# Optimization experiments

Hardware: AMD Instinct MI355X
Metric: run time of the kernel (lower is better)

The kernel has to match this reference:

```python
import jax, jax.numpy as jnp
import numpy as np

N_NODES = 50000
N_EDGES = 600000
N_GRAPHS = 64
D_NODE = 64
D_EDGE = 16
HID = 128
N_LAYERS = 3
LN_EPS = 1e-5


def setup_inputs() -> dict:
    key = jax.random.key(0)
    ks = jax.random.split(key, 16)
    inp = {
        'x': jax.random.normal(ks[0], (N_NODES, D_NODE), dtype=jnp.float32),
        'edge_index': jax.random.randint(ks[1], (2, N_EDGES), 0, N_NODES, dtype=jnp.int64),
        'edge_attr': jax.random.normal(ks[2], (N_EDGES, D_EDGE), dtype=jnp.float32),
        'batch': jnp.sort(jax.random.randint(ks[3], (N_NODES,), 0, N_GRAPHS, dtype=jnp.int64)),
    }
    def lin(k, fan_in, fan_out):
        bound = 1.0 / np.sqrt(fan_in)
        kw, kb = jax.random.split(k)
        w = jax.random.uniform(kw, (fan_in, fan_out), minval=-bound, maxval=bound, dtype=jnp.float32)
        b = jax.random.uniform(kb, (fan_out,), minval=-bound, maxval=bound, dtype=jnp.float32)
        return w, b
    inp['enc_w'], inp['enc_b'] = lin(ks[4], D_NODE, HID)
    inp['ln_g'] = jnp.ones((HID,), jnp.float32)
    inp['ln_b'] = jnp.zeros((HID,), jnp.float32)
    inp['edge_w'], inp['edge_b'] = lin(ks[5], D_EDGE, HID // 2)
    cw, cb = [], []
    for i in range(N_LAYERS):
        w, b = lin(ks[6 + i], HID, HID)
        cw.append(w); cb.append(b)
    inp['conv_ws'] = jnp.stack(cw)  # [L, HID, HID]
    inp['conv_bs'] = jnp.stack(cb)  # [L, HID]
    inp['c1_w'], inp['c1_b'] = lin(ks[10], HID, HID // 2)
    inp['c2_w'], inp['c2_b'] = lin(ks[11], HID // 2, 1)
    return inp


def _layernorm(h, g, b):
    mu = jnp.mean(h, axis=-1, keepdims=True)
    var = jnp.mean(jnp.square(h - mu), axis=-1, keepdims=True)
    return (h - mu) * jax.lax.rsqrt(var + LN_EPS) * g + b


def _gcn_forward(x, edge_attr, batch, src, dst,
                 enc_w, enc_b, ln_g, ln_b, edge_w, edge_b,
                 conv_ws, conv_bs, c1_w, c1_b, c2_w, c2_b):
    # node encoder: Linear -> ReLU -> LayerNorm
    h = _layernorm(jax.nn.relu(x @ enc_w + enc_b), ln_g, ln_b)
    # edge encoder (output unused downstream, kept for fidelity)
    _ = jax.nn.relu(edge_attr @ edge_w + edge_b)
    # GCN normalization with self-loops: deg = in-degree + 1
    deg = jax.ops.segment_sum(jnp.ones((src.shape[0],), h.dtype), dst, num_segments=N_NODES) + 1.0
    dis = jax.lax.rsqrt(deg)  # deg >= 1
    edge_norm = (dis[src] * dis[dst])[:, None]
    self_norm = (dis * dis)[:, None]  # 1/deg for self-loop
    for i in range(N_LAYERS):
        hw = h @ conv_ws[i]
        agg = jax.ops.segment_sum(hw[src] * edge_norm, dst, num_segments=N_NODES)
        h = agg + hw * self_norm + conv_bs[i]
        h = jax.nn.relu(h)  # dropout is identity at eval
    # global mean pool over graphs
    sums = jax.ops.segment_sum(h, batch, num_segments=N_GRAPHS)
    cnts = jax.ops.segment_sum(jnp.ones((h.shape[0],), h.dtype), batch, num_segments=N_GRAPHS)
    pooled = sums / jnp.maximum(cnts, 1.0)[:, None]
    # classifier: Linear -> ReLU -> (Dropout) -> Linear
    return jax.nn.relu(pooled @ c1_w + c1_b) @ c2_w + c2_b


def reference(x, edge_index, edge_attr, batch, enc_w, enc_b, ln_g, ln_b,
              edge_w, edge_b, conv_ws, conv_bs, c1_w, c1_b, c2_w, c2_b):
    src, dst = edge_index[0], edge_index[1]
    return _gcn_forward(x, edge_attr, batch, src, dst, enc_w, enc_b, ln_g, ln_b,
                        edge_w, edge_b, conv_ws, conv_bs, c1_w, c1_b, c2_w, c2_b)
```

## Files before the change

kernel.cpp:

```cpp
#include <hip/hip_runtime.h>

#define HID 128
#define DNODE 64
#define NNODES 50000
#define NEDGES 600000
#define NGRAPHS 64
#define LN_EPS 1e-5f

#define NBUCK 782
#define EPB 4096
#define BK1 ((NEDGES + EPB - 1) / EPB)

#define NZERO (NBUCK + NGRAPHS * HID)
#define NZERO4 ((NZERO + 3) / 4)
#define Z_BLKS ((NZERO4 + 255) / 256)
#define PKWC_BLKS (3 * 16384 / 256)
#define PKWE_BLKS (8192 / 256)
#define BND_BLKS ((NNODES + 255) / 256)

#define ENC_BLKS ((NNODES + 63) / 64)
#define E256_BLKS ((NEDGES + 255) / 256)

#define GC_BLKS (NNODES / 16)

typedef __attribute__((ext_vector_type(8))) short bf16x8;
typedef __attribute__((ext_vector_type(8))) unsigned short u16x8;
typedef __attribute__((ext_vector_type(4))) float f32x4;
typedef __attribute__((ext_vector_type(2))) float f32x2;

static __device__ __forceinline__ unsigned short f2bf(float f) {
  unsigned int u = __float_as_uint(f);
  u += 0x7fffu + ((u >> 16) & 1u);
  return (unsigned short)(u >> 16);
}
static __device__ __forceinline__ float bf2f(unsigned short h) {
  return __uint_as_float(((unsigned int)h) << 16);
}
static __device__ __forceinline__ void fp8x4_to_f32(unsigned int w, float* o) {
  f32x2 lo = __builtin_amdgcn_cvt_pk_f32_fp8(w, false);
  f32x2 hi = __builtin_amdgcn_cvt_pk_f32_fp8(w, true);
  o[0] = lo[0]; o[1] = lo[1]; o[2] = hi[0]; o[3] = hi[1];
}
static __device__ __forceinline__ unsigned int f32x4_to_fp8(float a, float b,
                                                            float c, float d) {
  unsigned int v = __builtin_amdgcn_cvt_pk_fp8_f32(a, b, 0, false);
  v = __builtin_amdgcn_cvt_pk_fp8_f32(c, d, v, true);
  return v;
}

__global__ void __launch_bounds__(256) prep0_kernel(
    int4* __restrict__ zp, const float* __restrict__ W,
    unsigned short* __restrict__ Wp, const float* __restrict__ enc_w,
    unsigned short* __restrict__ Wpe, const int* __restrict__ batch,
    int* __restrict__ gstart, int* __restrict__ gend) {
  int b = blockIdx.x;
  if (b < Z_BLKS) {
    int i = b * 256 + threadIdx.x;
    if (i < NZERO4) zp[i] = make_int4(0, 0, 0, 0);
  } else if (b < Z_BLKS + PKWC_BLKS) {
    int t = (b - Z_BLKS) * 256 + threadIdx.x;
    int i = t & 7;
    int lane = (t >> 3) & 63;
    int kk = (t >> 9) & 3;
    int nt = (t >> 11) & 7;
    int layer = t >> 14;
    int k = kk * 32 + (lane >> 4) * 8 + i;
    int n = nt * 16 + (lane & 15);
    Wp[t] = f2bf(W[((size_t)layer * HID + k) * HID + n]);
  } else if (b < Z_BLKS + PKWC_BLKS + PKWE_BLKS) {
    int t = (b - Z_BLKS - PKWC_BLKS) * 256 + threadIdx.x;
    int i = t & 7;
    int lane = (t >> 3) & 63;
    int kk = (t >> 9) & 1;
    int nt = (t >> 10) & 7;
    int k = kk * 32 + (lane >> 4) * 8 + i;
    int n = nt * 16 + (lane & 15);
    Wpe[t] = f2bf(enc_w[(size_t)k * HID + n]);
  } else {
    int i = (b - Z_BLKS - PKWC_BLKS - PKWE_BLKS) * 256 + threadIdx.x;
    if (i < NNODES) {
      int g = batch[i];
      if (i == 0 || batch[i - 1] != g) gstart[g] = i;
      if (i == NNODES - 1 || batch[i + 1] != g) gend[g] = i + 1;
    }
  }
}

__global__ void __launch_bounds__(256) prep1_kernel(
    const float* __restrict__ x, const unsigned short* __restrict__ Wpe,
    const unsigned short* __restrict__ Wp0, const float* __restrict__ enc_b,
    const float* __restrict__ ln_g, const float* __restrict__ ln_b,
    unsigned char* __restrict__ B1, const int* __restrict__ dst,
    int* __restrict__ gcount, unsigned int* __restrict__ bpos) {
  __shared__ __align__(16) unsigned short tile[4][16][136];
  __shared__ int lhist[NBUCK];
  int blk = blockIdx.x;
  if (blk < BK1) {
    int t = threadIdx.x;
    for (int i = t; i < NBUCK; i += 256) lhist[i] = 0;
    __syncthreads();
    int base = blk * EPB;
    int myd[16];
    int myr[16];
#pragma unroll
    for (int i = 0; i < 16; ++i) {
      int e = base + i * 256 + t;
      if (e < NEDGES) {
        int d = dst[e];
        myd[i] = d;
        myr[i] = atomicAdd(&lhist[d >> 6], 1);
      } else {
        myd[i] = -1;
        myr[i] = 0;
      }
    }
    __syncthreads();
    for (int i = t; i < NBUCK; i += 256) {
      int c = lhist[i];
      if (c) lhist[i] = atomicAdd(&gcount[i], c);
    }
    __syncthreads();
#pragma unroll
    for (int i = 0; i < 16; ++i) {
      if (myd[i] >= 0) {
        int e = base + i * 256 + t;
        bpos[e] = (unsigned int)(lhist[myd[i] >> 6] + myr[i]);
      }
    }
    return;
  }
  int b2 = blk - BK1;
  int wave = threadIdx.x >> 6;
  int lane = threadIdx.x & 63;
  int l15 = lane & 15, h = lane >> 4;
  int base = b2 * 64 + wave * 16;
  int row = base + l15;
  int rowc = row < NNODES ? row : NNODES - 1;
  const float* xr = x + (size_t)rowc * DNODE;
  bf16x8 a[2];
#pragma unroll
  for (int kk = 0; kk < 2; ++kk) {
    float4 p0 = *(const float4*)(xr + kk * 32 + h * 8);
    float4 p1 = *(const float4*)(xr + kk * 32 + h * 8 + 4);
    a[kk][0] = (short)f2bf(p0.x); a[kk][1] = (short)f2bf(p0.y);
    a[kk][2] = (short)f2bf(p0.z); a[kk][3] = (short)f2bf(p0.w);
    a[kk][4] = (short)f2bf(p1.x); a[kk][5] = (short)f2bf(p1.y);
    a[kk][6] = (short)f2bf(p1.z); a[kk][7] = (short)f2bf(p1.w);
  }
  f32x4 acc[8];
#pragma unroll
  for (int nt = 0; nt < 8; ++nt) acc[nt] = (f32x4)(0.f);
  const bf16x8* wp = (const bf16x8*)Wpe;
#pragma unroll
  for (int kk = 0; kk < 2; ++kk)
#pragma unroll
    for (int nt = 0; nt < 8; ++nt)
      acc[nt] = __builtin_amdgcn_mfma_f32_16x16x32_bf16(a[kk], wp[(nt * 2 + kk) * 64 + lane],
                                                        acc[nt], 0, 0, 0);
  float s[4] = {0.f, 0.f, 0.f, 0.f}, s2[4] = {0.f, 0.f, 0.f, 0.f};
#pragma unroll
  for (int nt = 0; nt < 8; ++nt) {
    float bcol = enc_b[nt * 16 + l15];
#pragma unroll
    for (int r = 0; r < 4; ++r) {
      float v = fmaxf(acc[nt][r] + bcol, 0.f);
      acc[nt][r] = v;
      s[r] += v;
      s2[r] = fmaf(v, v, s2[r]);
    }
  }
#pragma unroll
  for (int r = 0; r < 4; ++r) {
#pragma unroll
    for (int o = 1; o < 16; o <<= 1) {
      s[r] += __shfl_xor(s[r], o);
      s2[r] += __shfl_xor(s2[r], o);
    }
  }
  float mu[4], rstd[4];
#pragma unroll
  for (int r = 0; r < 4; ++r) {
    mu[r] = s[r] * (1.0f / HID);
    float var = s2[r] * (1.0f / HID) - mu[r] * mu[r];
    rstd[r] = rsqrtf(var + LN_EPS);
  }
#pragma unroll
  for (int nt = 0; nt < 8; ++nt) {
    float gcol = ln_g[nt * 16 + l15], bbcol = ln_b[nt * 16 + l15];
#pragma unroll
    for (int r = 0; r < 4; ++r)
      tile[wave][h * 4 + r][nt * 16 + l15] =
          f2bf((acc[nt][r] - mu[r]) * rstd[r] * gcol + bbcol);
  }
  __syncthreads();
  bf16x8 a2[4];
#pragma unroll
  for (int kk = 0; kk < 4; ++kk)
    a2[kk] = *(const bf16x8*)&tile[wave][l15][kk * 32 + h * 8];
  __syncthreads();
  f32x4 acc2[8];
#pragma unroll
  for (int nt = 0; nt < 8; ++nt) acc2[nt] = (f32x4)(0.f);
#pragma unroll
  for (int kk = 0; kk < 4; ++kk) {
#pragma unroll
    for (int nt = 0; nt < 8; ++nt) {
      bf16x8 wf = *(const bf16x8*)(Wp0 + (((nt * 4 + kk) * 64 + lane) << 3));
      acc2[nt] = __builtin_amdgcn_mfma_f32_16x16x32_bf16(a2[kk], wf, acc2[nt], 0, 0, 0);
    }
  }
#pragma unroll
  for (int nt = 0; nt < 8; ++nt)
#pragma unroll
    for (int r = 0; r < 4; ++r)
      tile[wave][h * 4 + r][nt * 16 + l15] = f2bf(acc2[nt][r]);
  __syncthreads();
  int trow = lane >> 2, tseg = lane & 3;
  int orow = base + trow;
  if (orow < NNODES) {
#pragma unroll
    for (int q = 0; q < 4; ++q) {
      u16x8 v = *(const u16x8*)&tile[wave][trow][tseg * 32 + q * 8];
      uint2 o;
      o.x = f32x4_to_fp8(bf2f((unsigned short)v[0]), bf2f((unsigned short)v[1]),
                         bf2f((unsigned short)v[2]), bf2f((unsigned short)v[3]));
      o.y = f32x4_to_fp8(bf2f((unsigned short)v[4]), bf2f((unsigned short)v[5]),
                         bf2f((unsigned short)v[6]), bf2f((unsigned short)v[7]));
      *(uint2*)(B1 + (size_t)orow * HID + tseg * 32 + q * 8) = o;
    }
  }
}

__global__ void __launch_bounds__(1024) scan_kernel(
    const int* __restrict__ gcount, int* __restrict__ boff,
    int* __restrict__ off) {
  __shared__ int s[1024];
  int t = threadIdx.x;
  int v = (t < NBUCK) ? gcount[t] : 0;
  s[t] = v;
  __syncthreads();
  for (int d = 1; d < 1024; d <<= 1) {
    int xv = (t >= d) ? s[t - d] : 0;
    __syncthreads();
    s[t] += xv;
    __syncthreads();
  }
  if (t < NBUCK) boff[t] = s[t] - v;
  if (t == 0) {
    boff[NBUCK] = s[1023];
    off[NNODES] = NEDGES;
  }
}

__global__ void __launch_bounds__(256) scat_kernel(
    const int* __restrict__ src, const int* __restrict__ dst,
    const unsigned int* __restrict__ bpos, const int* __restrict__ boff,
    unsigned int* __restrict__ sorted1) {
  int e = blockIdx.x * 256 + threadIdx.x;
  if (e >= NEDGES) return;
  int d = dst[e];
  unsigned int u = ((unsigned int)d << 16) | (unsigned int)src[e];
  sorted1[boff[d >> 6] + bpos[e]] = u;
}

__global__ void __launch_bounds__(1024) bucket_kernel(
    const int* __restrict__ boff, const unsigned int* __restrict__ sorted1,
    int* __restrict__ off, float* __restrict__ dis,
    unsigned int* __restrict__ epack) {
  __shared__ int h64[64];
  __shared__ int cur[64];
  int b = blockIdx.x, t = threadIdx.x;
  int lo = boff[b], hi = boff[b + 1];
  if (t < 64) h64[t] = 0;
  __syncthreads();
  for (int i = lo + t; i < hi; i += 1024)
    atomicAdd(&h64[(sorted1[i] >> 16) & 63], 1);
  __syncthreads();
  if (t == 0) {
    int run = 0;
    for (int j = 0; j < 64; ++j) {
      int c = h64[j];
      cur[j] = lo + run;
      int n = b * 64 + j;
      if (n < NNODES) {
        off[n] = lo + run;
        dis[n] = rsqrtf((float)c + 1.0f);
      }
      run += c;
    }
  }
  __syncthreads();
  for (int i = lo + t; i < hi; i += 1024) {
    unsigned int u = sorted1[i];
    int p = atomicAdd(&cur[(u >> 16) & 63], 1);
    epack[p] = u;
  }
}

__global__ void __launch_bounds__(256) norm_kernel(
    const float* __restrict__ dis, unsigned int* __restrict__ epack) {
  int e = blockIdx.x * 256 + threadIdx.x;
  if (e >= NEDGES) return;
  unsigned int u = epack[e];
  int d = u >> 16;
  int sN = u & 0xFFFFu;
  epack[e] = ((unsigned int)f2bf(dis[sN] * dis[d]) << 16) | (unsigned int)sN;
}

__global__ void __launch_bounds__(1024) gc_kernel(
    const int* __restrict__ off, const unsigned int* __restrict__ epack,
    const float* __restrict__ dis, const float* __restrict__ bias,
    const unsigned char* __restrict__ Bin, const unsigned short* __restrict__ Wnext,
    unsigned char* __restrict__ Bout) {
  __shared__ __align__(16) unsigned short As[16][136];
  __shared__ __align__(16) unsigned short Bs[16][136];
  int w = threadIdx.x >> 6, lane = threadIdx.x & 63;
  int n = blockIdx.x * 16 + w;
  int slot = lane >> 4, p = lane & 15;
  int lo = off[n], hi = off[n + 1];
  float acc0[8], acc1[8];
#pragma unroll
  for (int i = 0; i < 8; ++i) { acc0[i] = 0.f; acc1[i] = 0.f; }
  int idx = lo + slot;
  for (; idx + 4 < hi; idx += 8) {
    unsigned int e0 = epack[idx];
    unsigned int e1 = epack[idx + 4];
    float w0 = bf2f((unsigned short)(e0 >> 16));
    float w1 = bf2f((unsigned short)(e1 >> 16));
    uint2 v0 = *(const uint2*)(Bin + (size_t)(e0 & 0xFFFFu) * HID + p * 8);
    uint2 v1 = *(const uint2*)(Bin + (size_t)(e1 & 0xFFFFu) * HID + p * 8);
    float f0[8], f1[8];
    fp8x4_to_f32(v0.x, f0); fp8x4_to_f32(v0.y, f0 + 4);
    fp8x4_to_f32(v1.x, f1); fp8x4_to_f32(v1.y, f1 + 4);
#pragma unroll
    for (int i = 0; i < 8; ++i) acc0[i] = fmaf(f0[i], w0, acc0[i]);
#pragma unroll
    for (int i = 0; i < 8; ++i) acc1[i] = fmaf(f1[i], w1, acc1[i]);
  }
  if (idx < hi) {
    unsigned int e0 = epack[idx];
    float w0 = bf2f((unsigned short)(e0 >> 16));
    uint2 v0 = *(const uint2*)(Bin + (size_t)(e0 & 0xFFFFu) * HID + p * 8);
    float f0[8];
    fp8x4_to_f32(v0.x, f0); fp8x4_to_f32(v0.y, f0 + 4);
#pragma unroll
    for (int i = 0; i < 8; ++i) acc0[i] = fmaf(f0[i], w0, acc0[i]);
  }
#pragma unroll
  for (int i = 0; i < 8; ++i) {
    float a = acc0[i] + acc1[i];
    a += __shfl_xor(a, 16);
    a += __shfl_xor(a, 32);
    acc0[i] = a;
  }
  if (slot == 0) {
    float dn = dis[n];
    float d2 = dn * dn;
    uint2 sv = *(const uint2*)(Bin + (size_t)n * HID + p * 8);
    float sf[8];
    fp8x4_to_f32(sv.x, sf); fp8x4_to_f32(sv.y, sf + 4);
    float4 b0 = ((const float4*)bias)[p * 2];
    float4 b1 = ((const float4*)bias)[p * 2 + 1];
    float bb[8] = {b0.x, b0.y, b0.z, b0.w, b1.x, b1.y, b1.z, b1.w};
    u16x8 o;
#pragma unroll
    for (int i = 0; i < 8; ++i) {
      float v = fmaxf(fmaf(sf[i], d2, bb[i]) + acc0[i], 0.f);
      o[i] = (short)f2bf(v);
    }
    *(u16x8*)&As[w][p * 8] = o;
  }
  __syncthreads();
  if (w < 8) {
    bf16x8 a[4];
#pragma unroll
    for (int kk = 0; kk < 4; ++kk)
      a[kk] = *(const bf16x8*)&As[p][kk * 32 + slot * 8];
    f32x4 acc = (f32x4)(0.f);
#pragma unroll
    for (int kk = 0; kk < 4; ++kk) {
      bf16x8 wf = *(const bf16x8*)(Wnext + (((w * 4 + kk) * 64 + lane) << 3));
      acc = __builtin_amdgcn_mfma_f32_16x16x32_bf16(a[kk], wf, acc, 0, 0, 0);
    }
#pragma unroll
    for (int r = 0; r < 4; ++r)
      Bs[slot * 4 + r][w * 16 + p] = f2bf(acc[r]);
  }
  __syncthreads();
  if (threadIdx.x < 256) {
    int row = threadIdx.x >> 4, seg = threadIdx.x & 15;
    u16x8 v = *(const u16x8*)&Bs[row][seg * 8];
    uint2 o;
    o.x = f32x4_to_fp8(bf2f((unsigned short)v[0]), bf2f((unsigned short)v[1]),
                       bf2f((unsigned short)v[2]), bf2f((unsigned short)v[3]));
    o.y = f32x4_to_fp8(bf2f((unsigned short)v[4]), bf2f((unsigned short)v[5]),
                       bf2f((unsigned short)v[6]), bf2f((unsigned short)v[7]));
    *(uint2*)(Bout + (size_t)(blockIdx.x * 16 + row) * HID + seg * 8) = o;
  }
}

__global__ void __launch_bounds__(1024) g2pool_kernel(
    const int* __restrict__ off, const unsigned int* __restrict__ epack,
    const float* __restrict__ dis, const float* __restrict__ bias,
    const unsigned char* __restrict__ Bin, const int* __restrict__ batch,
    float* __restrict__ sums) {
  __shared__ float Ps[16][132];
  __shared__ int bg[16];
  int w = threadIdx.x >> 6, lane = threadIdx.x & 63;
  int n = blockIdx.x * 16 + w;
  int slot = lane >> 4, p = lane & 15;
  int lo = off[n], hi = off[n + 1];
  float acc0[8], acc1[8];
#pragma unroll
  for (int i = 0; i < 8; ++i) { acc0[i] = 0.f; acc1[i] = 0.f; }
  int idx = lo + slot;
  for (; idx + 4 < hi; idx += 8) {
    unsigned int e0 = epack[idx];
    unsigned int e1 = epack[idx + 4];
    float w0 = bf2f((unsigned short)(e0 >> 16));
    float w1 = bf2f((unsigned short)(e1 >> 16));
    uint2 v0 = *(const uint2*)(Bin + (size_t)(e0 & 0xFFFFu) * HID + p * 8);
    uint2 v1 = *(const uint2*)(Bin + (size_t)(e1 & 0xFFFFu) * HID + p * 8);
    float f0[8], f1[8];
    fp8x4_to_f32(v0.x, f0); fp8x4_to_f32(v0.y, f0 + 4);
    fp8x4_to_f32(v1.x, f1); fp8x4_to_f32(v1.y, f1 + 4);
#pragma unroll
    for (int i = 0; i < 8; ++i) acc0[i] = fmaf(f0[i], w0, acc0[i]);
#pragma unroll
    for (int i = 0; i < 8; ++i) acc1[i] = fmaf(f1[i], w1, acc1[i]);
  }
  if (idx < hi) {
    unsigned int e0 = epack[idx];
    float w0 = bf2f((unsigned short)(e0 >> 16));
    uint2 v0 = *(const uint2*)(Bin + (size_t)(e0 & 0xFFFFu) * HID + p * 8);
    float f0[8];
    fp8x4_to_f32(v0.x, f0); fp8x4_to_f32(v0.y, f0 + 4);
#pragma unroll
    for (int i = 0; i < 8; ++i) acc0[i] = fmaf(f0[i], w0, acc0[i]);
  }
#pragma unroll
  for (int i = 0; i < 8; ++i) {
    float a = acc0[i] + acc1[i];
    a += __shfl_xor(a, 16);
    a += __shfl_xor(a, 32);
    acc0[i] = a;
  }
  if (slot == 0) {
    float dn = dis[n];
    float d2 = dn * dn;
    uint2 sv = *(const uint2*)(Bin + (size_t)n * HID + p * 8);
    float sf[8];
    fp8x4_to_f32(sv.x, sf); fp8x4_to_f32(sv.y, sf + 4);
    float4 b0 = ((const float4*)bias)[p * 2];
    float4 b1 = ((const float4*)bias)[p * 2 + 1];
    float bb[8] = {b0.x, b0.y, b0.z, b0.w, b1.x, b1.y, b1.z, b1.w};
    float4 o0, o1;
    o0.x = fmaxf(fmaf(sf[0], d2, bb[0]) + acc0[0], 0.f);
    o0.y = fmaxf(fmaf(sf[1], d2, bb[1]) + acc0[1], 0.f);
    o0.z = fmaxf(fmaf(sf[2], d2, bb[2]) + acc0[2], 0.f);
    o0.w = fmaxf(fmaf(sf[3], d2, bb[3]) + acc0[3], 0.f);
    o1.x = fmaxf(fmaf(sf[4], d2, bb[4]) + acc0[4], 0.f);
    o1.y = fmaxf(fmaf(sf[5], d2, bb[5]) + acc0[5], 0.f);
    o1.z = fmaxf(fmaf(sf[6], d2, bb[6]) + acc0[6], 0.f);
    o1.w = fmaxf(fmaf(sf[7], d2, bb[7]) + acc0[7], 0.f);
    *(float4*)&Ps[w][p * 8] = o0;
    *(float4*)&Ps[w][p * 8 + 4] = o1;
  }
  if (threadIdx.x < 16) bg[threadIdx.x] = batch[blockIdx.x * 16 + threadIdx.x];
  __syncthreads();
  if (threadIdx.x < HID) {
    int j = threadIdx.x;
    float a = 0.f;
    int cur = bg[0];
    for (int r = 0; r < 16; ++r) {
      int g = bg[r];
      if (g != cur) { atomicAdd(&sums[cur * HID + j], a); a = 0.f; cur = g; }
      a += Ps[r][j];
    }
    atomicAdd(&sums[cur * HID + j], a);
  }
}

__global__ void __launch_bounds__(64) cls_kernel(
    const float* __restrict__ sums, const int* __restrict__ gstart,
    const int* __restrict__ gend, const float* __restrict__ c1w,
    const float* __restrict__ c1b, const float* __restrict__ c2w,
    const float* __restrict__ c2b, float* __restrict__ out) {
  int g = blockIdx.x;
  int j = threadIdx.x;
  __shared__ float pooled[HID];
  float cnt = (float)(gend[g] - gstart[g]);
  float inv = 1.0f / fmaxf(cnt, 1.0f);
  pooled[j] = sums[g * HID + j] * inv;
  pooled[j + 64] = sums[g * HID + j + 64] * inv;
  __syncthreads();
  float s = c1b[j];
#pragma unroll 8
  for (int k = 0; k < HID; ++k) s = fmaf(pooled[k], c1w[k * 64 + j], s);
  s = fmaxf(s, 0.f) * c2w[j];
#pragma unroll
  for (int off = 32; off; off >>= 1) s += __shfl_down(s, off);
  if (j == 0) out[g] = s + c2b[0];
}

extern "C" void kernel_launch(void* const* d_in, const int* in_sizes, int n_in,
                              void* d_out, int out_size, void* d_ws, size_t ws_size,
                              hipStream_t stream) {
  const float* x = (const float*)d_in[0];
  const int* edge_index = (const int*)d_in[1];
  const int* batch = (const int*)d_in[3];
  const float* enc_w = (const float*)d_in[4];
  const float* enc_b = (const float*)d_in[5];
  const float* ln_g = (const float*)d_in[6];
  const float* ln_b = (const float*)d_in[7];
  const float* conv_ws = (const float*)d_in[10];
  const float* conv_bs = (const float*)d_in[11];
  const float* c1w = (const float*)d_in[12];
  const float* c1b = (const float*)d_in[13];
  const float* c2w = (const float*)d_in[14];
  const float* c2b = (const float*)d_in[15];
  float* out = (float*)d_out;

  unsigned char* B1 = (unsigned char*)d_ws;
  unsigned char* B2 = B1 + (size_t)NNODES * HID;
  unsigned short* Wp = (unsigned short*)(B2 + (size_t)NNODES * HID);
  unsigned short* Wpe = Wp + 3 * 16384;
  unsigned int* epack = (unsigned int*)(Wpe + 8192);
  unsigned int* sorted1 = epack + NEDGES;
  unsigned int* bpos = sorted1 + NEDGES;
  int* gcount = (int*)(bpos + NEDGES);
  float* sums = (float*)(gcount + NBUCK);
  int* boff = (int*)(sums + NGRAPHS * HID);
  int* off = boff + NBUCK + 1;
  float* dis = (float*)(off + NNODES + 1);
  int* gstart = (int*)(dis + NNODES);
  int* gend = gstart + NGRAPHS;

  const int* srcp = edge_index;
  const int* dstp = edge_index + NEDGES;

  prep0_kernel<<<Z_BLKS + PKWC_BLKS + PKWE_BLKS + BND_BLKS, 256, 0, stream>>>(
      (int4*)gcount, conv_ws, Wp, enc_w, Wpe, batch, gstart, gend);
  prep1_kernel<<<BK1 + ENC_BLKS, 256, 0, stream>>>(
      x, Wpe, Wp, enc_b, ln_g, ln_b, B1, dstp, gcount, bpos);
  scan_kernel<<<1, 1024, 0, stream>>>(gcount, boff, off);
  scat_kernel<<<E256_BLKS, 256, 0, stream>>>(srcp, dstp, bpos, boff, sorted1);
  bucket_kernel<<<NBUCK, 1024, 0, stream>>>(boff, sorted1, off, dis, epack);
  norm_kernel<<<E256_BLKS, 256, 0, stream>>>(dis, epack);

  gc_kernel<<<GC_BLKS, 1024, 0, stream>>>(off, epack, dis, conv_bs, B1,
                                          Wp + (size_t)1 * 16384, B2);
  gc_kernel<<<GC_BLKS, 1024, 0, stream>>>(off, epack, dis, conv_bs + HID, B2,
                                          Wp + (size_t)2 * 16384, B1);
  g2pool_kernel<<<GC_BLKS, 1024, 0, stream>>>(off, epack, dis, conv_bs + 2 * HID,
                                              B1, batch, sums);
  cls_kernel<<<NGRAPHS, 64, 0, stream>>>(sums, gstart, gend, c1w, c1b, c2w, c2b, out);
}
```

Measured before the change: 158.5 us.

## Fold bucket scan into scatter and split bucket kernel to fuse edge norm

Removes the single-block scan kernel. Each scatter block now recomputes the bucket prefix sum itself from gcount in shared memory, and bucketA computes its own base with a reduction. The old bucket kernel is split in two: bucketA builds per-node offsets and inverse-sqrt degrees, and bucketB places edges and writes the bf16 edge normalisation directly, which removes the separate norm pass. This cuts launches and one full pass over epack, at the cost of redundant scan and reduction work in every block.

```diff
diff --git a/kernel.cpp b/kernel.cpp
--- a/kernel.cpp
+++ b/kernel.cpp
@@ -52,8 +52,9 @@
     int4* __restrict__ zp, const float* __restrict__ W,
     unsigned short* __restrict__ Wp, const float* __restrict__ enc_w,
     unsigned short* __restrict__ Wpe, const int* __restrict__ batch,
-    int* __restrict__ gstart, int* __restrict__ gend) {
+    int* __restrict__ gstart, int* __restrict__ gend, int* __restrict__ off) {
   int b = blockIdx.x;
+  if (b == 0 && threadIdx.x == 0) off[NNODES] = NEDGES;
   if (b < Z_BLKS) {
     int i = b * 256 + threadIdx.x;
     if (i < NZERO4) zp[i] = make_int4(0, 0, 0, 0);
@@ -231,80 +232,102 @@
   }
 }
 
-__global__ void __launch_bounds__(1024) scan_kernel(
-    const int* __restrict__ gcount, int* __restrict__ boff,
-    int* __restrict__ off) {
-  __shared__ int s[1024];
-  int t = threadIdx.x;
-  int v = (t < NBUCK) ? gcount[t] : 0;
-  s[t] = v;
-  __syncthreads();
-  for (int d = 1; d < 1024; d <<= 1) {
-    int xv = (t >= d) ? s[t - d] : 0;
-    __syncthreads();
-    s[t] += xv;
-    __syncthreads();
-  }
-  if (t < NBUCK) boff[t] = s[t] - v;
-  if (t == 0) {
-    boff[NBUCK] = s[1023];
-    off[NNODES] = NEDGES;
-  }
-}
-
 __global__ void __launch_bounds__(256) scat_kernel(
     const int* __restrict__ src, const int* __restrict__ dst,
-    const unsigned int* __restrict__ bpos, const int* __restrict__ boff,
+    const unsigned int* __restrict__ bpos, const int* __restrict__ gcount,
     unsigned int* __restrict__ sorted1) {
-  int e = blockIdx.x * 256 + threadIdx.x;
+  __shared__ int bofs[1024];
+  __shared__ int tsum[256];
+  int t = threadIdx.x;
+  int g[4];
+  int s = 0;
+#pragma unroll
+  for (int i = 0; i < 4; ++i) {
+    int idx = 4 * t + i;
+    g[i] = (idx < NBUCK) ? gcount[idx] : 0;
+    s += g[i];
+  }
+  tsum[t] = s;
+  __syncthreads();
+  for (int d = 1; d < 256; d <<= 1) {
+    int v = (t >= d) ? tsum[t - d] : 0;
+    __syncthreads();
+    tsum[t] += v;
+    __syncthreads();
+  }
+  int run = tsum[t] - s;
+#pragma unroll
+  for (int i = 0; i < 4; ++i) {
+    bofs[4 * t + i] = run;
+    run += g[i];
+  }
+  __syncthreads();
+  int e = blockIdx.x * 256 + t;
   if (e >= NEDGES) return;
   int d = dst[e];
-  unsigned int u = ((unsigned int)d << 16) | (unsigned int)src[e];
-  sorted1[boff[d >> 6] + bpos[e]] = u;
-}
-
-__global__ void __launch_bounds__(1024) bucket_kernel(
-    const int* __restrict__ boff, const unsigned int* __restrict__ sorted1,
-    int* __restrict__ off, float* __restrict__ dis,
-    unsigned int* __restrict__ epack) {
+  sorted1[bofs[d >> 6] + bpos[e]] =
+      ((unsigned int)d << 16) | (unsigned int)src[e];
+}
+
+__global__ void __launch_bounds__(256) bucketA_kernel(
+    const int* __restrict__ gcount, const unsigned int* __restrict__ sorted1,
+    int* __restrict__ off, float* __restrict__ dis) {
   __shared__ int h64[64];
+  __shared__ int red[256];
+  int b = blockIdx.x, t = threadIdx.x;
+  int partial = 0;
+  for (int i = t; i < b; i += 256) partial += gcount[i];
+  red[t] = partial;
+  __syncthreads();
+  for (int d = 128; d; d >>= 1) {
+    if (t < d) red[t] += red[t + d];
+    __syncthreads();
+  }
+  int base = red[0];
+  int cnt = gcount[b];
+  if (t < 64) h64[t] = 0;
+  __syncthreads();
+  for (int i = base + t; i < base + cnt; i += 256)
+    atomicAdd(&h64[(sorted1[i] >> 16) & 63], 1);
+  __syncthreads();
+  if (t < 64) {
+    int own = h64[t];
+    int x = own;
+#pragma unroll
+    for (int o = 1; o < 64; o <<= 1) {
+      int v = __shfl_up(x, o);
+      if (t >= o) x += v;
+    }
+    int n = b * 64 + t;
+    if (n < NNODES) {
+      off[n] = base + (x - own);
+      dis[n] = rsqrtf((float)own + 1.0f);
+    }
+  }
+}
+
+__global__ void __launch_bounds__(256) bucketB_kernel(
+    const int* __restrict__ off, const float* __restrict__ dis,
+    const unsigned int* __restrict__ sorted1, unsigned int* __restrict__ epack) {
   __shared__ int cur[64];
+  __shared__ float disl[64];
   int b = blockIdx.x, t = threadIdx.x;
-  int lo = boff[b], hi = boff[b + 1];
-  if (t < 64) h64[t] = 0;
-  __syncthreads();
-  for (int i = lo + t; i < hi; i += 1024)
-    atomicAdd(&h64[(sorted1[i] >> 16) & 63], 1);
-  __syncthreads();
-  if (t == 0) {
-    int run = 0;
-    for (int j = 0; j < 64; ++j) {
-      int c = h64[j];
-      cur[j] = lo + run;
-      int n = b * 64 + j;
-      if (n < NNODES) {
-        off[n] = lo + run;
-        dis[n] = rsqrtf((float)c + 1.0f);
-      }
-      run += c;
-    }
-  }
-  __syncthreads();
-  for (int i = lo + t; i < hi; i += 1024) {
+  if (t < 64) {
+    int n = b * 64 + t;
+    cur[t] = (n < NNODES) ? off[n] : NEDGES;
+    disl[t] = (n < NNODES) ? dis[n] : 1.0f;
+  }
+  __syncthreads();
+  int base = cur[0];
+  int end = (b == NBUCK - 1) ? NEDGES : off[(b + 1) * 64];
+  for (int i = base + t; i < end; i += 256) {
     unsigned int u = sorted1[i];
-    int p = atomicAdd(&cur[(u >> 16) & 63], 1);
-    epack[p] = u;
-  }
-}
-
-__global__ void __launch_bounds__(256) norm_kernel(
-    const float* __restrict__ dis, unsigned int* __restrict__ epack) {
-  int e = blockIdx.x * 256 + threadIdx.x;
-  if (e >= NEDGES) return;
-  unsigned int u = epack[e];
-  int d = u >> 16;
-  int sN = u & 0xFFFFu;
-  epack[e] = ((unsigned int)f2bf(dis[sN] * dis[d]) << 16) | (unsigned int)sN;
+    int d63 = (u >> 16) & 63;
+    int sN = u & 0xFFFFu;
+    int p = atomicAdd(&cur[d63], 1);
+    float wgt = dis[sN] * disl[d63];
+    epack[p] = ((unsigned int)f2bf(wgt) << 16) | (unsigned int)sN;
+  }
 }
 
 __global__ void __launch_bounds__(1024) gc_kernel(
@@ -530,8 +553,7 @@
   unsigned int* bpos = sorted1 + NEDGES;
   int* gcount = (int*)(bpos + NEDGES);
   float* sums = (float*)(gcount + NBUCK);
-  int* boff = (int*)(sums + NGRAPHS * HID);
-  int* off = boff + NBUCK + 1;
+  int* off = (int*)(sums + NGRAPHS * HID);
   float* dis = (float*)(off + NNODES + 1);
   int* gstart = (int*)(dis + NNODES);
   int* gend = gstart + NGRAPHS;
@@ -540,13 +562,12 @@
   const int* dstp = edge_index + NEDGES;
 
   prep0_kernel<<<Z_BLKS + PKWC_BLKS + PKWE_BLKS + BND_BLKS, 256, 0, stream>>>(
-      (int4*)gcount, conv_ws, Wp, enc_w, Wpe, batch, gstart, gend);
+      (int4*)gcount, conv_ws, Wp, enc_w, Wpe, batch, gstart, gend, off);
   prep1_kernel<<<BK1 + ENC_BLKS, 256, 0, stream>>>(
       x, Wpe, Wp, enc_b, ln_g, ln_b, B1, dstp, gcount, bpos);
-  scan_kernel<<<1, 1024, 0, stream>>>(gcount, boff, off);
-  scat_kernel<<<E256_BLKS, 256, 0, stream>>>(srcp, dstp, bpos, boff, sorted1);
-  bucket_kernel<<<NBUCK, 1024, 0, stream>>>(boff, sorted1, off, dis, epack);
-  norm_kernel<<<E256_BLKS, 256, 0, stream>>>(dis, epack);
+  scat_kernel<<<E256_BLKS, 256, 0, stream>>>(srcp, dstp, bpos, gcount, sorted1);
+  bucketA_kernel<<<NBUCK, 256, 0, stream>>>(gcount, sorted1, off, dis);
+  bucketB_kernel<<<NBUCK, 256, 0, stream>>>(off, dis, sorted1, epack);
 
   gc_kernel<<<GC_BLKS, 1024, 0, stream>>>(off, epack, dis, conv_bs, B1,
                                           Wp + (size_t)1 * 16384, B2);
```

Result: faster. 149.1 us (-6.0%).
